# Kernel tuning notes

Measured on AMD Instinct MI355X. Metric: run time of the kernel, lower is better.

Reference implementation:

```python
import jax, jax.numpy as jnp
import numpy as np

B, T, H = 32, 1000, 512


def setup_inputs() -> dict:
    key = jax.random.key(0)
    k1, k2, k3, k4, k5 = jax.random.split(key, 5)
    return {
        "wx": jax.random.normal(k1, (B, T, 4 * H), dtype=jnp.float32),
        "u": jax.random.normal(k2, (4 * H, H), dtype=jnp.float32) * (1.0 / np.sqrt(H)),
        "u_bias": jax.random.normal(k3, (4 * H,), dtype=jnp.float32) * 0.1,
        "ht": jax.random.normal(k4, (B, H), dtype=jnp.float32),
        "ct": jax.random.normal(k5, (B, H), dtype=jnp.float32),
    }


def reference(wx, u, u_bias, ht, ct):
    # wx: [B, T, 4H]; scan over time with sequential (ht, ct) state.
    def step(carry, wx_t):
        h, c = carry
        gates = wx_t + h @ u.T + u_bias          # [B, 4H]
        it, ft, gt, ot = jnp.split(gates, 4, axis=1)
        it = jax.nn.sigmoid(it)
        ft = jax.nn.sigmoid(ft)
        gt = jnp.tanh(gt)
        ot = jax.nn.sigmoid(ot)
        c = ft * c + it * gt
        h = ot * jnp.tanh(c)
        return (h, c), (h, c, it, ft, gt, ot)

    wx_t = jnp.swapaxes(wx, 0, 1)                # [T, B, 4H]
    _, (h, c, it, ft, gt, ot) = jax.lax.scan(step, (ht, ct), wx_t)
    # each is [T, B, H] -> [B, T, H]
    tr = lambda a: jnp.swapaxes(a, 0, 1)
    return tr(h), tr(c), tr(it), tr(ft), tr(gt), tr(ot)
```

## Files before the change

kernel.cpp:

```cpp
#include <hip/hip_runtime.h>

#define BB 32
#define TT 1000
#define HH 512
#define G4 2048
#define BTH ((size_t)BB * TT * HH)

typedef short short8 __attribute__((ext_vector_type(8)));
typedef float f32x4 __attribute__((ext_vector_type(4)));

__device__ __forceinline__ unsigned short f2bf(float f) {
    union { float f; unsigned u; } v; v.f = f;
    unsigned r = v.u + 0x7FFF + ((v.u >> 16) & 1);
    return (unsigned short)(r >> 16);
}

#define RING_WORDS (2 * 8 * 32 * 64)

__global__ void lstm_init_ring(unsigned* ring) {
    int i = blockIdx.x * 256 + threadIdx.x;
    __hip_atomic_store(ring + i, 0xFFFFFFFFu, __ATOMIC_RELAXED,
                       __HIP_MEMORY_SCOPE_AGENT);
}

#define LDS_BAR() do {                                      \
    asm volatile("s_waitcnt lgkmcnt(0)" ::: "memory");      \
    __builtin_amdgcn_s_barrier();                           \
    asm volatile("" ::: "memory");                          \
    __builtin_amdgcn_sched_barrier(0);                      \
} while (0)

__global__ void __launch_bounds__(256, 1)
lstm_main(const float* __restrict__ wx, const float* __restrict__ u,
          const float* __restrict__ ub, const float* __restrict__ ht0,
          const float* __restrict__ ct0, float* __restrict__ out,
          unsigned* __restrict__ ring)
{
    __shared__ __align__(16) unsigned short lds_h[16 * 512];
    __shared__ float lds_gates[4 * 64];

    const int tid  = threadIdx.x;
    const int bid  = blockIdx.x;
    const int cg   = bid & 31;
    const int qb   = bid >> 5;
    const int lane = tid & 63;
    const int wv   = tid >> 6;

    for (int j = 0; j < 3; ++j) {
        int idx8 = tid + j * 256;
        int r = 4 + (idx8 >> 6);
        int k = (idx8 & 63) * 8;
        short8 z = {0, 0, 0, 0, 0, 0, 0, 0};
        *(short8*)&lds_h[(r * 512 + k) ^ ((r & 7) << 3)] = z;
    }
    {
        int r = wv, k = lane * 8;
        const float* src = ht0 + (size_t)(qb * 4 + r) * HH + k;
        float4 v0 = *(const float4*)src;
        float4 v1 = *(const float4*)(src + 4);
        union { short8 v8; unsigned short s[8]; } p;
        p.s[0] = f2bf(v0.x); p.s[1] = f2bf(v0.y); p.s[2] = f2bf(v0.z); p.s[3] = f2bf(v0.w);
        p.s[4] = f2bf(v1.x); p.s[5] = f2bf(v1.y); p.s[6] = f2bf(v1.z); p.s[7] = f2bf(v1.w);
        *(short8*)&lds_h[(r * 512 + k) ^ ((r & 7) << 3)] = p.v8;
    }

    const int arow = lane & 15, ahi = lane >> 4;
    short8 breg[16];
    {
        const float* bp = u + (size_t)(wv * HH + cg * 16 + arow) * HH + ahi * 8;
#pragma unroll
        for (int kk = 0; kk < 16; ++kk) {
            float4 v0 = *(const float4*)(bp + kk * 32);
            float4 v1 = *(const float4*)(bp + kk * 32 + 4);
            union { short8 v8; unsigned short s[8]; } p;
            p.s[0] = f2bf(v0.x); p.s[1] = f2bf(v0.y); p.s[2] = f2bf(v0.z); p.s[3] = f2bf(v0.w);
            p.s[4] = f2bf(v1.x); p.s[5] = f2bf(v1.y); p.s[6] = f2bf(v1.z); p.s[7] = f2bf(v1.w);
            breg[kk] = p.v8;
        }
    }

    const int gate = lane >> 4;
    const int jc   = lane & 15;
    const float bias_r = ub[gate * HH + cg * 16 + jc];

    float c_reg = 0.f;
    if (lane < 16)
        c_reg = ct0[(size_t)(qb * 4 + wv) * HH + cg * 16 + lane];

    const size_t wx0 = (size_t)(qb * 4 + wv) * TT * G4 + gate * HH + cg * 16 + jc;
    float wx_cur = wx[wx0];
    float wx_nxt = wx[wx0 + G4];

    const size_t ob_gate = (size_t)(2 + gate) * BTH +
                           (size_t)(qb * 4 + wv) * TT * HH + cg * 16 + jc;
    const size_t ob_h = (size_t)(qb * 4 + wv) * TT * HH + cg * 16 + lane;

    const int a_off = arow * 512 + ahi * 8;
    const int a_msk = (arow & 7) << 3;

    const int myp = tid >> 3;
    const int mw  = (tid & 7) * 8;
    const int mb  = mw >> 4;
    const int mj  = mw & 15;

    __syncthreads();

    for (int t = 0; t < TT; ++t) {
        if (t > 0 && myp != cg) {
            const unsigned long long* src = (const unsigned long long*)
                (ring + ((size_t)((t - 1) & 1) * 8 + qb) * 2048 + myp * 64 + mw);
            const unsigned tg = (unsigned)(t - 1);
            const unsigned long long want =
                (unsigned long long)tg | ((unsigned long long)tg << 32);
            const unsigned long long msk = 0x0000FFFF0000FFFFull;
            unsigned long long q0, q1, q2, q3;
            for (;;) {
                q0 = __hip_atomic_load(src + 0, __ATOMIC_RELAXED, __HIP_MEMORY_SCOPE_AGENT);
                q1 = __hip_atomic_load(src + 1, __ATOMIC_RELAXED, __HIP_MEMORY_SCOPE_AGENT);
                q2 = __hip_atomic_load(src + 2, __ATOMIC_RELAXED, __HIP_MEMORY_SCOPE_AGENT);
                q3 = __hip_atomic_load(src + 3, __ATOMIC_RELAXED, __HIP_MEMORY_SCOPE_AGENT);
                if (((q0 & msk) == want) & ((q1 & msk) == want) &
                    ((q2 & msk) == want) & ((q3 & msk) == want)) break;
            }
            union { short8 v8; unsigned u[4]; } pv;
            pv.u[0] = ((unsigned)(q0 >> 16) & 0xFFFFu) | ((unsigned)(q0 >> 48) << 16);
            pv.u[1] = ((unsigned)(q1 >> 16) & 0xFFFFu) | ((unsigned)(q1 >> 48) << 16);
            pv.u[2] = ((unsigned)(q2 >> 16) & 0xFFFFu) | ((unsigned)(q2 >> 48) << 16);
            pv.u[3] = ((unsigned)(q3 >> 16) & 0xFFFFu) | ((unsigned)(q3 >> 48) << 16);
            *(short8*)&lds_h[(mb * 512 + myp * 16 + mj) ^ ((mb & 7) << 3)] = pv.v8;
        }
        LDS_BAR();

        const float wx_use = wx_cur;
        wx_cur = wx_nxt;

        f32x4 acc0 = {0.f, 0.f, 0.f, 0.f}, acc1 = {0.f, 0.f, 0.f, 0.f};
        f32x4 acc2 = {0.f, 0.f, 0.f, 0.f}, acc3 = {0.f, 0.f, 0.f, 0.f};
#pragma unroll
        for (int kk = 0; kk < 4; ++kk) {
            short8 a0 = *(const short8*)&lds_h[(a_off + kk * 32) ^ a_msk];
            short8 a1 = *(const short8*)&lds_h[(a_off + (kk + 4) * 32) ^ a_msk];
            short8 a2 = *(const short8*)&lds_h[(a_off + (kk + 8) * 32) ^ a_msk];
            short8 a3 = *(const short8*)&lds_h[(a_off + (kk + 12) * 32) ^ a_msk];
            acc0 = __builtin_amdgcn_mfma_f32_16x16x32_bf16(a0, breg[kk],      acc0, 0, 0, 0);
            acc1 = __builtin_amdgcn_mfma_f32_16x16x32_bf16(a1, breg[kk + 4],  acc1, 0, 0, 0);
            acc2 = __builtin_amdgcn_mfma_f32_16x16x32_bf16(a2, breg[kk + 8],  acc2, 0, 0, 0);
            acc3 = __builtin_amdgcn_mfma_f32_16x16x32_bf16(a3, breg[kk + 12], acc3, 0, 0, 0);
        }
        f32x4 g = (acc0 + acc1) + (acc2 + acc3);
        if (lane < 16) {
#pragma unroll
            for (int rr = 0; rr < 4; ++rr)
                lds_gates[rr * 64 + wv * 16 + lane] = g[rr];
        }
        LDS_BAR();

        float gv = lds_gates[wv * 64 + lane] + wx_use + bias_r;
        float xs = (gate == 2) ? 2.f * gv : gv;
        float s  = 1.f / (1.f + __expf(-xs));
        float act = (gate == 2) ? 2.f * s - 1.f : s;

        float af = __shfl(act, (lane & 15) + 16, 64);
        float ag = __shfl(act, (lane & 15) + 32, 64);
        float ao = __shfl(act, (lane & 15) + 48, 64);
        if (lane < 16) {
            c_reg = af * c_reg + act * ag;
            float e2 = __expf(-2.f * c_reg);
            float th = 2.f / (1.f + e2) - 1.f;
            float hn = ao * th;
            unsigned short hb = f2bf(hn);
            unsigned pk = ((unsigned)hb << 16) | (unsigned)t;
            __hip_atomic_store(ring + ((size_t)(t & 1) * 8 + qb) * 2048 +
                                   cg * 64 + wv * 16 + lane,
                               pk, __ATOMIC_RELAXED, __HIP_MEMORY_SCOPE_AGENT);
            lds_h[(wv * 512 + cg * 16 + lane) ^ ((wv & 7) << 3)] = hb;
            out[ob_h + (size_t)t * HH] = hn;
            out[BTH + ob_h + (size_t)t * HH] = c_reg;
        }
        out[ob_gate + (size_t)t * HH] = act;

        asm volatile("" ::: "memory");
        if (t + 2 < TT) wx_nxt = wx[wx0 + (size_t)(t + 2) * G4];
    }
}

extern "C" void kernel_launch(void* const* d_in, const int* in_sizes, int n_in,
                              void* d_out, int out_size, void* d_ws, size_t ws_size,
                              hipStream_t stream) {
    const float* wx = (const float*)d_in[0];
    const float* u  = (const float*)d_in[1];
    const float* ub = (const float*)d_in[2];
    const float* ht = (const float*)d_in[3];
    const float* ct = (const float*)d_in[4];
    float* out = (float*)d_out;
    unsigned* ring = (unsigned*)d_ws;

    lstm_init_ring<<<RING_WORDS / 256, 256, 0, stream>>>(ring);

    void* args[] = {(void*)&wx, (void*)&u, (void*)&ub, (void*)&ht,
                    (void*)&ct, (void*)&out, (void*)&ring};
    hipLaunchCooperativeKernel((void*)lstm_main, dim3(256), dim3(256), args, 0, stream);
}
```

Before: 2.028 ms.

## Remap blocks across XCDs and add a dual-ring exchange with XCD-local polling

The block-to-(batch,column) mapping is swapped so that blocks sharing a batch group (qb) land on the same XCD under round-robin dispatch. Each h value is now written to two rings: one through sc0 stores meant to stay XCD-local, and one through agent-scope atomic stores. Consumers poll the local ring with sc0 loads for a few tries before falling back to the global ring. The goal is to cut cross-XCD coherence latency in the per-step spin-wait. The change also halves the MFMA accumulator chains, moves the wx prefetch earlier, and replaces the custom LDS barrier with __syncthreads. The cost is a second store per element and a dependence on the XCD placement assumption for the local ring to be visible.

Result: slower. 2.777 ms (+36.9%).

```diff
diff --git a/kernel.cpp b/kernel.cpp
--- a/kernel.cpp
+++ b/kernel.cpp
@@ -34,15 +34,15 @@
 lstm_main(const float* __restrict__ wx, const float* __restrict__ u,
           const float* __restrict__ ub, const float* __restrict__ ht0,
           const float* __restrict__ ct0, float* __restrict__ out,
-          unsigned* __restrict__ ring)
+          unsigned* __restrict__ gring, unsigned* __restrict__ lring)
 {
     __shared__ __align__(16) unsigned short lds_h[16 * 512];
     __shared__ float lds_gates[4 * 64];
 
     const int tid  = threadIdx.x;
     const int bid  = blockIdx.x;
-    const int cg   = bid & 31;
-    const int qb   = bid >> 5;
+    const int qb   = bid & 7;
+    const int cg   = bid >> 3;
     const int lane = tid & 63;
     const int wv   = tid >> 6;
 
@@ -107,20 +107,35 @@
 
     for (int t = 0; t < TT; ++t) {
         if (t > 0 && myp != cg) {
-            const unsigned long long* src = (const unsigned long long*)
-                (ring + ((size_t)((t - 1) & 1) * 8 + qb) * 2048 + myp * 64 + mw);
+            const unsigned base = ((unsigned)((t - 1) & 1) * 8 + (unsigned)qb) * 2048
+                                  + myp * 64 + mw;
+            const unsigned long long* gsrc = (const unsigned long long*)(gring + base);
+            const unsigned long long* lsrc = (const unsigned long long*)(lring + base);
             const unsigned tg = (unsigned)(t - 1);
             const unsigned long long want =
                 (unsigned long long)tg | ((unsigned long long)tg << 32);
             const unsigned long long msk = 0x0000FFFF0000FFFFull;
             unsigned long long q0, q1, q2, q3;
+            int tries = 0;
             for (;;) {
-                q0 = __hip_atomic_load(src + 0, __ATOMIC_RELAXED, __HIP_MEMORY_SCOPE_AGENT);
-                q1 = __hip_atomic_load(src + 1, __ATOMIC_RELAXED, __HIP_MEMORY_SCOPE_AGENT);
-                q2 = __hip_atomic_load(src + 2, __ATOMIC_RELAXED, __HIP_MEMORY_SCOPE_AGENT);
-                q3 = __hip_atomic_load(src + 3, __ATOMIC_RELAXED, __HIP_MEMORY_SCOPE_AGENT);
+                if (tries < 8) {
+                    asm volatile(
+                        "global_load_dwordx2 %0, %4, off sc0\n\t"
+                        "global_load_dwordx2 %1, %4, off offset:8 sc0\n\t"
+                        "global_load_dwordx2 %2, %4, off offset:16 sc0\n\t"
+                        "global_load_dwordx2 %3, %4, off offset:24 sc0\n\t"
+                        "s_waitcnt vmcnt(0)"
+                        : "=&v"(q0), "=&v"(q1), "=&v"(q2), "=&v"(q3)
+                        : "v"(lsrc) : "memory");
+                } else {
+                    q0 = __hip_atomic_load(gsrc + 0, __ATOMIC_RELAXED, __HIP_MEMORY_SCOPE_AGENT);
+                    q1 = __hip_atomic_load(gsrc + 1, __ATOMIC_RELAXED, __HIP_MEMORY_SCOPE_AGENT);
+                    q2 = __hip_atomic_load(gsrc + 2, __ATOMIC_RELAXED, __HIP_MEMORY_SCOPE_AGENT);
+                    q3 = __hip_atomic_load(gsrc + 3, __ATOMIC_RELAXED, __HIP_MEMORY_SCOPE_AGENT);
+                }
                 if (((q0 & msk) == want) & ((q1 & msk) == want) &
                     ((q2 & msk) == want) & ((q3 & msk) == want)) break;
+                ++tries;
             }
             union { short8 v8; unsigned u[4]; } pv;
             pv.u[0] = ((unsigned)(q0 >> 16) & 0xFFFFu) | ((unsigned)(q0 >> 48) << 16);
@@ -129,25 +144,21 @@
             pv.u[3] = ((unsigned)(q3 >> 16) & 0xFFFFu) | ((unsigned)(q3 >> 48) << 16);
             *(short8*)&lds_h[(mb * 512 + myp * 16 + mj) ^ ((mb & 7) << 3)] = pv.v8;
         }
-        LDS_BAR();
+        __syncthreads();
 
         const float wx_use = wx_cur;
         wx_cur = wx_nxt;
+        if (t + 2 < TT) wx_nxt = wx[wx0 + (size_t)(t + 2) * G4];
 
         f32x4 acc0 = {0.f, 0.f, 0.f, 0.f}, acc1 = {0.f, 0.f, 0.f, 0.f};
-        f32x4 acc2 = {0.f, 0.f, 0.f, 0.f}, acc3 = {0.f, 0.f, 0.f, 0.f};
 #pragma unroll
-        for (int kk = 0; kk < 4; ++kk) {
-            short8 a0 = *(const short8*)&lds_h[(a_off + kk * 32) ^ a_msk];
-            short8 a1 = *(const short8*)&lds_h[(a_off + (kk + 4) * 32) ^ a_msk];
-            short8 a2 = *(const short8*)&lds_h[(a_off + (kk + 8) * 32) ^ a_msk];
-            short8 a3 = *(const short8*)&lds_h[(a_off + (kk + 12) * 32) ^ a_msk];
-            acc0 = __builtin_amdgcn_mfma_f32_16x16x32_bf16(a0, breg[kk],      acc0, 0, 0, 0);
-            acc1 = __builtin_amdgcn_mfma_f32_16x16x32_bf16(a1, breg[kk + 4],  acc1, 0, 0, 0);
-            acc2 = __builtin_amdgcn_mfma_f32_16x16x32_bf16(a2, breg[kk + 8],  acc2, 0, 0, 0);
-            acc3 = __builtin_amdgcn_mfma_f32_16x16x32_bf16(a3, breg[kk + 12], acc3, 0, 0, 0);
-        }
-        f32x4 g = (acc0 + acc1) + (acc2 + acc3);
+        for (int kk = 0; kk < 8; ++kk) {
+            short8 va0 = *(const short8*)&lds_h[(a_off + kk * 32) ^ a_msk];
+            short8 va1 = *(const short8*)&lds_h[(a_off + (kk + 8) * 32) ^ a_msk];
+            acc0 = __builtin_amdgcn_mfma_f32_16x16x32_bf16(va0, breg[kk], acc0, 0, 0, 0);
+            acc1 = __builtin_amdgcn_mfma_f32_16x16x32_bf16(va1, breg[kk + 8], acc1, 0, 0, 0);
+        }
+        f32x4 g = acc0 + acc1;
         if (lane < 16) {
 #pragma unroll
             for (int rr = 0; rr < 4; ++rr)
@@ -170,17 +181,17 @@
             float hn = ao * th;
             unsigned short hb = f2bf(hn);
             unsigned pk = ((unsigned)hb << 16) | (unsigned)t;
-            __hip_atomic_store(ring + ((size_t)(t & 1) * 8 + qb) * 2048 +
-                                   cg * 64 + wv * 16 + lane,
-                               pk, __ATOMIC_RELAXED, __HIP_MEMORY_SCOPE_AGENT);
+            const unsigned pb = ((unsigned)(t & 1) * 8 + (unsigned)qb) * 2048 +
+                                cg * 64 + wv * 16 + lane;
+            asm volatile("global_store_dword %0, %1, off sc0"
+                         :: "v"(lring + pb), "v"(pk) : "memory");
+            __hip_atomic_store(gring + pb, pk, __ATOMIC_RELAXED,
+                               __HIP_MEMORY_SCOPE_AGENT);
             lds_h[(wv * 512 + cg * 16 + lane) ^ ((wv & 7) << 3)] = hb;
             out[ob_h + (size_t)t * HH] = hn;
             out[BTH + ob_h + (size_t)t * HH] = c_reg;
         }
         out[ob_gate + (size_t)t * HH] = act;
-
-        asm volatile("" ::: "memory");
-        if (t + 2 < TT) wx_nxt = wx[wx0 + (size_t)(t + 2) * G4];
     }
 }
 
@@ -193,11 +204,14 @@
     const float* ht = (const float*)d_in[3];
     const float* ct = (const float*)d_in[4];
     float* out = (float*)d_out;
-    unsigned* ring = (unsigned*)d_ws;
-
-    lstm_init_ring<<<RING_WORDS / 256, 256, 0, stream>>>(ring);
+    unsigned* gring = (unsigned*)d_ws;
+    const int dual = (ws_size >= (size_t)2 * RING_WORDS * 4);
+    unsigned* lring = dual ? (gring + RING_WORDS) : gring;
+    const int init_words = dual ? 2 * RING_WORDS : RING_WORDS;
+
+    lstm_init_ring<<<init_words / 256, 256, 0, stream>>>(gring);
 
     void* args[] = {(void*)&wx, (void*)&u, (void*)&ub, (void*)&ht,
-                    (void*)&ct, (void*)&out, (void*)&ring};
+                    (void*)&ct, (void*)&out, (void*)&gring, (void*)&lring};
     hipLaunchCooperativeKernel((void*)lstm_main, dim3(256), dim3(256), args, 0, stream);
 }
```
